# Kernel optimization log

Measured on AMD Instinct MI355X. Metric: run time of the kernel, lower is better.

Reference implementation:

```python
import jax, jax.numpy as jnp
import numpy as np

# ---- static config (matches init_kwargs) ----
B, N_CAMS, C, H, W = 2, 6, 256, 32, 88
BEV_H = BEV_W = 100
NQ = BEV_H * BEV_W
D_PILLAR = 4
HEADS = 8
LEVELS = 3
HEAD_DIM = C // HEADS
PC_RANGE = (-51.2, -51.2, -5.0, 51.2, 51.2, 3.0)
OGFH, OGFW = 256, 704


def _make_lidar2img():
    """Plausible lidar->image projection matrices (K @ [R|t]) for 6 ring cameras."""
    mats = np.zeros((B, N_CAMS, 4, 4), np.float32)
    K = np.array([[557.0, 0.0, OGFW / 2.0], [0.0, 557.0, OGFH / 2.0], [0.0, 0.0, 1.0]], np.float64)
    for b in range(B):
        for n in range(N_CAMS):
            yaw = 2.0 * np.pi * n / N_CAMS + 0.05 * b
            fwd = np.array([np.cos(yaw), np.sin(yaw), 0.0])
            right = np.array([np.sin(yaw), -np.cos(yaw), 0.0])
            down = np.array([0.0, 0.0, -1.0])
            R = np.stack([right, down, fwd])  # lidar -> camera axes
            cam_center = np.array([1.5 * np.cos(yaw), 1.5 * np.sin(yaw), 1.8])
            t = -R @ cam_center
            P = K @ np.concatenate([R, t[:, None]], axis=1)
            mats[b, n, :3, :] = P.astype(np.float32)
            mats[b, n, 3, 3] = 1.0
    return jnp.asarray(mats)


def setup_inputs() -> dict:
    key = jax.random.key(0)
    ks = jax.random.split(key, 16)
    s = 0.02
    return {
        'imgs': jax.random.normal(ks[0], (B, N_CAMS, C, H, W), jnp.float32),
        'lidar2img': _make_lidar2img(),
        'bev_query': jax.random.normal(ks[1], (NQ, 1, C), jnp.float32) * s,
        'bev_pos': jax.random.normal(ks[2], (1, NQ, C), jnp.float32) * s,
        'cams_embeds': jax.random.normal(ks[3], (N_CAMS, C), jnp.float32) * s,
        'level_embeds': jax.random.normal(ks[4], (LEVELS, C), jnp.float32) * s,
        'w_fpn': jax.random.normal(ks[5], (LEVELS, C, C), jnp.float32) * s,
        'b_fpn': jnp.zeros((LEVELS, C), jnp.float32),
        'w_value': jax.random.normal(ks[6], (C, C), jnp.float32) * s,
        'b_value': jnp.zeros((C,), jnp.float32),
        'w_off': jax.random.normal(ks[7], (C, HEADS * LEVELS * D_PILLAR * 2), jnp.float32) * s,
        'b_off': jax.random.normal(ks[8], (HEADS * LEVELS * D_PILLAR * 2,), jnp.float32) * 0.5,
        'w_attn': jax.random.normal(ks[9], (C, HEADS * LEVELS * D_PILLAR), jnp.float32) * s,
        'b_attn': jnp.zeros((HEADS * LEVELS * D_PILLAR,), jnp.float32),
        'w_out': jax.random.normal(ks[10], (C, C), jnp.float32) * s,
        'b_out': jnp.zeros((C,), jnp.float32),
        'w_ts1': jax.random.normal(ks[11], (C, C), jnp.float32) * s,
        'b_ts1': jnp.zeros((C,), jnp.float32),
        'w_ts2': jax.random.normal(ks[12], (C, C), jnp.float32) * s,
        'b_ts2': jnp.zeros((C,), jnp.float32),
    }


def _deform_sample(v, loc, h, w):
    """Bilinear sample (grid_sample, zero padding, align_corners=False).
    v: [N, heads, h*w, dh]; loc: [N, heads, Q, 2] normalized to [0,1]. -> [N, heads, Q, dh]"""
    x = loc[..., 0] * w - 0.5
    y = loc[..., 1] * h - 0.5
    x0 = jnp.floor(x)
    y0 = jnp.floor(y)
    out = jnp.zeros(v.shape[:2] + (loc.shape[2], v.shape[-1]), v.dtype)
    for dx in (0, 1):
        for dy in (0, 1):
            xi = x0 + dx
            yi = y0 + dy
            wgt = (1.0 - jnp.abs(x - xi)) * (1.0 - jnp.abs(y - yi))
            valid = (xi >= 0) & (xi < w) & (yi >= 0) & (yi < h)
            idx = (jnp.clip(yi, 0, h - 1) * w + jnp.clip(xi, 0, w - 1)).astype(jnp.int32)
            g = jnp.take_along_axis(v, idx[..., None], axis=2)
            out = out + g * (wgt * valid)[..., None]
    return out


def _forward(imgs, lidar2img, bev_query, bev_pos, cams_embeds, level_embeds,
             w_fpn, b_fpn, w_value, b_value, w_off, b_off, w_attn, b_attn,
             w_out, b_out, w_ts1, b_ts1, w_ts2, b_ts2):
    # ---- FPN: 3 levels at strides 1/2/4 with per-level 1x1 projection ----
    x = imgs.reshape(B * N_CAMS, C, H, W)
    feats, shapes = [], []
    cur = x
    for l in range(LEVELS):
        if l > 0:
            bn, c, h, w = cur.shape
            cur = cur.reshape(bn, c, h // 2, 2, w // 2, 2).mean(axis=(3, 5))
        f = jnp.einsum('bchw,cd->bdhw', cur, w_fpn[l]) + b_fpn[l][None, :, None, None]
        feats.append(f)
        shapes.append((f.shape[2], f.shape[3]))
    # ---- flatten levels + cam/level embeds: [N, sum_hw, B, C] ----
    flat = []
    for l, f in enumerate(feats):
        h, w = shapes[l]
        fl = jnp.transpose(f.reshape(B, N_CAMS, C, h * w), (1, 0, 3, 2))  # [N,B,hw,C]
        fl = fl + cams_embeds[:, None, None, :] + level_embeds[l][None, None, None, :]
        flat.append(fl)
    feat_flatten = jnp.transpose(jnp.concatenate(flat, axis=2), (0, 2, 1, 3))  # [N,sum_hw,B,C]

    # ---- 3D pillar reference points, normalized [0,1] ----
    zrange = PC_RANGE[5] - PC_RANGE[2]
    zs = jnp.linspace(0.5, zrange - 0.5, D_PILLAR) / zrange
    xs = (jnp.arange(BEV_W, dtype=jnp.float32) + 0.5) / BEV_W
    ys = (jnp.arange(BEV_H, dtype=jnp.float32) + 0.5) / BEV_H
    gy, gx = jnp.meshgrid(ys, xs, indexing='ij')
    ref2d = jnp.stack([gx.ravel(), gy.ravel()], axis=-1)  # [NQ,2]
    ref3d = jnp.concatenate([
        jnp.broadcast_to(ref2d[None], (D_PILLAR, NQ, 2)),
        jnp.broadcast_to(zs[:, None, None].astype(jnp.float32), (D_PILLAR, NQ, 1)),
    ], axis=-1)
    scale = jnp.array([PC_RANGE[3] - PC_RANGE[0], PC_RANGE[4] - PC_RANGE[1], zrange], jnp.float32)
    shift = jnp.array(PC_RANGE[:3], jnp.float32)
    xyz = ref3d * scale + shift
    homog = jnp.concatenate([xyz, jnp.ones((D_PILLAR, NQ, 1), jnp.float32)], axis=-1)

    # ---- point sampling: project to each camera, mask invalid pixels ----
    pts = jnp.einsum('bnij,dqj->nbqdi', lidar2img, homog)  # [N,B,NQ,D,4]
    eps = 1e-5
    depth = pts[..., 2]
    xy = pts[..., :2] / jnp.maximum(depth[..., None], eps)
    ref_cam = xy / jnp.array([OGFW, OGFH], jnp.float32)  # [N,B,NQ,D,2]
    bev_mask = ((depth > eps) & (ref_cam[..., 0] > 0) & (ref_cam[..., 0] < 1)
                & (ref_cam[..., 1] > 0) & (ref_cam[..., 1] < 1))  # [N,B,NQ,D]

    pos = bev_pos[0]  # [NQ,C]

    def sca(query, value, ref_b, mask_b):
        # query [NQ,C]; value [N,sum_hw,C]; ref_b [N,NQ,D,2]; mask_b [N,NQ,D]
        residual = query
        q = query + pos
        v = value @ w_value + b_value
        off = (q @ w_off + b_off).reshape(NQ, HEADS, LEVELS, D_PILLAR, 2)
        attn = jax.nn.softmax((q @ w_attn + b_attn).reshape(NQ, HEADS, LEVELS * D_PILLAR), axis=-1)
        attn = attn.reshape(NQ, HEADS, LEVELS, D_PILLAR)
        out = jnp.zeros((N_CAMS, NQ, HEADS, HEAD_DIM), q.dtype)
        start = 0
        for l, (h, w) in enumerate(shapes):
            hw = h * w
            v_l = jnp.transpose(v[:, start:start + hw].reshape(N_CAMS, hw, HEADS, HEAD_DIM), (0, 2, 1, 3))
            start += hw
            norm = jnp.array([w, h], q.dtype)
            loc = ref_b[:, :, None, :, :] + off[None, :, :, l] / norm  # [N,NQ,heads,D,2]
            loc = jnp.transpose(loc, (0, 2, 1, 3, 4)).reshape(N_CAMS, HEADS, NQ * D_PILLAR, 2)
            s = _deform_sample(v_l, loc, h, w).reshape(N_CAMS, HEADS, NQ, D_PILLAR, HEAD_DIM)
            out = out + jnp.einsum('nhqpd,qhp->nqhd', s, attn[:, :, l])
        out = out.reshape(N_CAMS, NQ, C)
        valid = mask_b.any(axis=-1)  # [N,NQ]
        slots = (out * valid[..., None].astype(out.dtype)).sum(axis=0)
        count = jnp.maximum(valid.sum(axis=0), 1).astype(out.dtype)[:, None]
        slots = slots / count
        return slots @ w_out + b_out + residual

    def tsblock(t):
        return jax.nn.relu(t @ w_ts1 + b_ts1) @ w_ts2 + b_ts2

    bq = jnp.transpose(bev_query, (1, 0, 2))[0]  # [NQ,C]
    groups = []
    ego = bq
    for b in range(B):
        val = feat_flatten[:, :, b, :]
        r = ref_cam[:, b]
        m = bev_mask[:, b]
        if b == 0:
            for _ in range(2):
                bq = tsblock(sca(bq, val, r, m))
            ego = bq
            groups.append(ego.reshape(C, BEV_W, BEV_H))
        else:
            nb = tsblock(sca(ego, val, r, m))
            groups.append(nb.reshape(C, BEV_W, BEV_H))
    bev_groups = jnp.stack(groups, axis=0)  # [B,C,BEV_W,BEV_H]
    return bq[None], bev_groups


def reference(imgs, lidar2img, bev_query, bev_pos, cams_embeds, level_embeds,
              w_fpn, b_fpn, w_value, b_value, w_off, b_off, w_attn, b_attn,
              w_out, b_out, w_ts1, b_ts1, w_ts2, b_ts2):
    return _forward(imgs, lidar2img, bev_query, bev_pos, cams_embeds, level_embeds,
                    w_fpn, b_fpn, w_value, b_value, w_off, b_off, w_attn, b_attn,
                    w_out, b_out, w_ts1, b_ts1, w_ts2, b_ts2)
```

## Files before the change

### kernel.cpp

```cpp
#include <hip/hip_runtime.h>
#include <math.h>

typedef __attribute__((ext_vector_type(8))) short bf16x8;
typedef __attribute__((ext_vector_type(4))) float f32x4;

__device__ __forceinline__ unsigned short f2bf(float x) {
  union { float f; unsigned int u; } v; v.f = x;
  unsigned int r = v.u + 0x7fffu + ((v.u >> 16) & 1u);
  return (unsigned short)(r >> 16);
}
__device__ __forceinline__ float bf2f(unsigned short b) {
  union { unsigned int u; float f; } v; v.u = ((unsigned int)b) << 16; return v.f;
}
__device__ __forceinline__ void split2(float x, unsigned short& h, unsigned short& l) {
  h = f2bf(x);
  l = f2bf(x - bf2f(h));
}
__device__ __forceinline__ int fsi(int q, int c) { return q * 256 + (c ^ ((q & 7) << 2)); }

__device__ __forceinline__ void ld16(const unsigned short* b, bf16x8* f) {
  const unsigned short* b1 = b + 2048;
  const unsigned short* b2 = b + 4096;
  const unsigned short* b3 = b + 6144;
  asm volatile(
    "global_load_dwordx4 %0, %16, off\n\t"
    "global_load_dwordx4 %1, %16, off offset:1024\n\t"
    "global_load_dwordx4 %2, %16, off offset:2048\n\t"
    "global_load_dwordx4 %3, %16, off offset:3072\n\t"
    "global_load_dwordx4 %4, %17, off\n\t"
    "global_load_dwordx4 %5, %17, off offset:1024\n\t"
    "global_load_dwordx4 %6, %17, off offset:2048\n\t"
    "global_load_dwordx4 %7, %17, off offset:3072\n\t"
    "global_load_dwordx4 %8, %18, off\n\t"
    "global_load_dwordx4 %9, %18, off offset:1024\n\t"
    "global_load_dwordx4 %10, %18, off offset:2048\n\t"
    "global_load_dwordx4 %11, %18, off offset:3072\n\t"
    "global_load_dwordx4 %12, %19, off\n\t"
    "global_load_dwordx4 %13, %19, off offset:1024\n\t"
    "global_load_dwordx4 %14, %19, off offset:2048\n\t"
    "global_load_dwordx4 %15, %19, off offset:3072\n\t"
    "s_waitcnt vmcnt(0)"
    : "=&v"(f[0]), "=&v"(f[1]), "=&v"(f[2]), "=&v"(f[3]),
      "=&v"(f[4]), "=&v"(f[5]), "=&v"(f[6]), "=&v"(f[7]),
      "=&v"(f[8]), "=&v"(f[9]), "=&v"(f[10]), "=&v"(f[11]),
      "=&v"(f[12]), "=&v"(f[13]), "=&v"(f[14]), "=&v"(f[15])
    : "v"(b), "v"(b1), "v"(b2), "v"(b3));
}

#define MFMA(a, b, c) __builtin_amdgcn_mfma_f32_16x16x32_bf16(a, b, c, 0, 0, 0)

__device__ __forceinline__ void gemm2tiles(
    const unsigned short* __restrict__ Wp, int tile0,
    int lane, int lk, int l15,
    const unsigned short (&AS)[2][32][32][8], f32x4 (&acc)[2][2])
{
  const unsigned short* base = Wp + ((size_t)(tile0 >> 1) * 16384) + (size_t)lane * 8;
  bf16x8 f[32];
  ld16(base, f);
  ld16(base + 8192, f + 16);
#pragma unroll
  for (int ks = 0; ks < 8; ++ks) {
    bf16x8 bqh0 = *(const bf16x8*)&AS[0][ks * 4 + lk][l15][0];
    bf16x8 bqh1 = *(const bf16x8*)&AS[0][ks * 4 + lk][16 + l15][0];
    bf16x8 bql0 = *(const bf16x8*)&AS[1][ks * 4 + lk][l15][0];
    bf16x8 bql1 = *(const bf16x8*)&AS[1][ks * 4 + lk][16 + l15][0];
    bf16x8 h0 = f[2 * ks], l0 = f[2 * ks + 1];
    bf16x8 h1 = f[16 + 2 * ks], l1 = f[17 + 2 * ks];
    acc[0][0] = MFMA(h0, bqh0, acc[0][0]);
    acc[0][0] = MFMA(h0, bql0, acc[0][0]);
    acc[0][0] = MFMA(l0, bqh0, acc[0][0]);
    acc[0][1] = MFMA(h0, bqh1, acc[0][1]);
    acc[0][1] = MFMA(h0, bql1, acc[0][1]);
    acc[0][1] = MFMA(l0, bqh1, acc[0][1]);
    acc[1][0] = MFMA(h1, bqh0, acc[1][0]);
    acc[1][0] = MFMA(h1, bql0, acc[1][0]);
    acc[1][0] = MFMA(l1, bqh0, acc[1][0]);
    acc[1][1] = MFMA(h1, bqh1, acc[1][1]);
    acc[1][1] = MFMA(h1, bql1, acc[1][1]);
    acc[1][1] = MFMA(l1, bqh1, acc[1][1]);
  }
}

__device__ __forceinline__ void gemm1tile(
    const unsigned short* __restrict__ Wp, int tile,
    int lane, int lk, int l15,
    const unsigned short (&AS)[2][32][32][8], f32x4 (&acc)[2])
{
  const unsigned short* base = Wp + ((size_t)(tile >> 1) * 16384) + (size_t)(tile & 1) * 8192 + (size_t)lane * 8;
  bf16x8 f[16];
  ld16(base, f);
#pragma unroll
  for (int ks = 0; ks < 8; ++ks) {
    bf16x8 bqh0 = *(const bf16x8*)&AS[0][ks * 4 + lk][l15][0];
    bf16x8 bqh1 = *(const bf16x8*)&AS[0][ks * 4 + lk][16 + l15][0];
    bf16x8 bql0 = *(const bf16x8*)&AS[1][ks * 4 + lk][l15][0];
    bf16x8 bql1 = *(const bf16x8*)&AS[1][ks * 4 + lk][16 + l15][0];
    bf16x8 eh = f[2 * ks], el = f[2 * ks + 1];
    acc[0] = MFMA(eh, bqh0, acc[0]);
    acc[0] = MFMA(eh, bql0, acc[0]);
    acc[0] = MFMA(el, bqh0, acc[0]);
    acc[1] = MFMA(eh, bqh1, acc[1]);
    acc[1] = MFMA(eh, bql1, acc[1]);
    acc[1] = MFMA(el, bqh1, acc[1]);
  }
}

__global__ __launch_bounds__(256) void pool2x2(const float* __restrict__ in, float* __restrict__ out,
                                               int h, int w, int total)
{
  int i = blockIdx.x * 256 + threadIdx.x;
  if (i >= total) return;
  int x = i % w; int r = i / w; int y = r % h; int ci = r / h;
  const float* p = in + (size_t)ci * (4 * h * w) + (size_t)(2 * y) * (2 * w) + 2 * x;
  out[i] = (p[0] + p[1] + p[2 * w] + p[2 * w + 1]) * 0.25f;
}

__global__ __launch_bounds__(256) void prep(
    const float* __restrict__ wo, const float* __restrict__ bo,
    const float* __restrict__ wa, const float* __restrict__ ba,
    const float* __restrict__ wout, const float* __restrict__ wts1, const float* __restrict__ wts2,
    const float* __restrict__ wfpn, const float* __restrict__ wval,
    const float* __restrict__ cams, const float* __restrict__ lev,
    const float* __restrict__ bfpn, const float* __restrict__ bval,
    unsigned short* __restrict__ wcatH, unsigned short* __restrict__ wcatL, float* __restrict__ bcat,
    unsigned short* __restrict__ woutH, unsigned short* __restrict__ woutL,
    unsigned short* __restrict__ wts1H, unsigned short* __restrict__ wts1L,
    unsigned short* __restrict__ w45H, unsigned short* __restrict__ w45L,
    unsigned short* __restrict__ wcombH, unsigned short* __restrict__ wcombL,
    float* __restrict__ e2)
{
  int bb = blockIdx.x, t = threadIdx.x;
  if (bb < 768) {
    int l = bb >> 8, i = bb & 255, j = t;
    const float* a = wfpn + ((size_t)l * 256 + i) * 256;
    float acc = 0.f;
    for (int k = 0; k < 256; ++k) acc = fmaf(a[k], wval[(size_t)k * 256 + j], acc);
    unsigned short h, lo; split2(acc, h, lo);
    size_t o = ((size_t)l * 256 + j) * 256 + i;
    wcombH[o] = h; wcombL[o] = lo;
  } else if (bb < 1056) {
    int i = (bb - 768) * 256 + t;
    int c = i >> 8, k = i & 255;
    float v = (c < 192) ? wo[k * 192 + c] : wa[k * 96 + (c - 192)];
    unsigned short h, l; split2(v, h, l);
    wcatH[i] = h; wcatL[i] = l;
    if (i < 288) bcat[i] = (i < 192) ? bo[i] : ba[i - 192];
  } else if (bb < 1312) {
    int i = (bb - 1056) * 256 + t;
    int nn = i >> 8, k = i & 255;
    float v = wout[(size_t)k * 256 + nn];
    unsigned short h, l; split2(v, h, l);
    woutH[i] = h; woutL[i] = l;
  } else if (bb < 1568) {
    int i = (bb - 1312) * 256 + t;
    int nn = i >> 8, k = i & 255;
    float v = wts1[(size_t)k * 256 + nn];
    unsigned short h, l; split2(v, h, l);
    wts1H[i] = h; wts1L[i] = l;
  } else if (bb < 1824) {
    int i = (bb - 1568) * 256 + t;
    int nn = i >> 8, k = i & 255;
    float v = wts2[(size_t)k * 256 + nn];
    unsigned short h, l; split2(v, h, l);
    w45H[i] = h; w45L[i] = l;
  } else if (bb < 2112) {
    int mp = bb - 1824;
    int k = t;
    float acc = 0.f;
    for (int j = 0; j < 256; ++j) {
      float wc = (mp < 192) ? wo[j * 192 + mp] : wa[j * 96 + (mp - 192)];
      acc = fmaf(wts2[(size_t)k * 256 + j], wc, acc);
    }
    unsigned short h, l; split2(acc, h, l);
    size_t o = (size_t)(256 + mp) * 256 + k;
    w45H[o] = h; w45L[o] = l;
  } else {
    int e = bb - 2112;
    int n = e / 3, l = e % 3, j = t;
    float acc = bval[j];
    for (int k = 0; k < 256; ++k) {
      float s = cams[n * 256 + k] + lev[l * 256 + k] + bfpn[l * 256 + k];
      acc = fmaf(s, wval[(size_t)k * 256 + j], acc);
    }
    e2[(size_t)e * 256 + j] = acc;
  }
}

__global__ __launch_bounds__(256) void relayout(
    const unsigned short* __restrict__ wcombH, const unsigned short* __restrict__ wcombL,
    const unsigned short* __restrict__ wcatH, const unsigned short* __restrict__ wcatL,
    const unsigned short* __restrict__ woutH, const unsigned short* __restrict__ woutL,
    const unsigned short* __restrict__ wts1H, const unsigned short* __restrict__ wts1L,
    const unsigned short* __restrict__ w45H, const unsigned short* __restrict__ w45L,
    unsigned short* __restrict__ wcombP, unsigned short* __restrict__ wcatP,
    unsigned short* __restrict__ woutP, unsigned short* __restrict__ wts1P,
    unsigned short* __restrict__ w45P)
{
  int bb = blockIdx.x, t = threadIdx.x;
  const unsigned short *H, *L; unsigned short* P; int tile;
  if (bb < 48)      { H = wcombH; L = wcombL; P = wcombP; tile = bb; }
  else if (bb < 66) { H = wcatH;  L = wcatL;  P = wcatP;  tile = bb - 48; }
  else if (bb < 82) { H = woutH;  L = woutL;  P = woutP;  tile = bb - 66; }
  else if (bb < 98) { H = wts1H;  L = wts1L;  P = wts1P;  tile = bb - 82; }
  else              { H = w45H;   L = w45L;   P = w45P;   tile = bb - 98; }
#pragma unroll
  for (int e = 0; e < 32; ++e) {
    int idx = t * 32 + e;
    int slot = idx >> 9;
    int lane = (idx >> 3) & 63;
    int j8 = idx & 7;
    int ks = slot >> 1, hl = slot & 1;
    int col = tile * 16 + (lane & 15);
    int k = ks * 32 + (lane >> 4) * 8 + j8;
    size_t dst = ((size_t)(tile >> 1) * 16384) + (size_t)(((tile & 1) << 4) + slot) * 512 + (size_t)lane * 8 + j8;
    P[dst] = (hl ? L : H)[(size_t)col * 256 + k];
  }
}

__global__ __launch_bounds__(512) void value_fused(
    const float* __restrict__ img0, const float* __restrict__ cur1, const float* __restrict__ cur2,
    const unsigned short* __restrict__ wcombP,
    const float* __restrict__ e2, float* __restrict__ V)
{
  __shared__ __align__(16) unsigned short AS[2][32][32][8];
  int t = threadIdx.x, wid = t >> 6, lane = t & 63, l15 = lane & 15, lk = lane >> 4;
  int bx = blockIdx.x, cam = blockIdx.y;
  int level, tb, hw; const float* src;
  if (bx < 88)       { level = 0; tb = bx;       hw = 2816; src = img0; }
  else if (bx < 110) { level = 1; tb = bx - 88;  hw = 704;  src = cur1; }
  else               { level = 2; tb = bx - 110; hw = 176;  src = cur2; }
  int p0 = tb * 32;
  const int LST[3] = {0, 2816, 3520};
  src += (size_t)cam * 256 * hw;

  {
    int f4g = t & 7, kb = t >> 3;
    bool full = (p0 + 32 <= hw);
#pragma unroll
    for (int j = 0; j < 4; ++j) {
      int k = kb + j * 64;
      const float* row = src + (size_t)k * hw;
      int p = p0 + 4 * f4g;
      float4 v;
      if (full) v = *(const float4*)(row + p);
      else {
        v.x = (p < hw) ? row[p] : 0.f;     v.y = (p + 1 < hw) ? row[p + 1] : 0.f;
        v.z = (p + 2 < hw) ? row[p + 2] : 0.f; v.w = (p + 3 < hw) ? row[p + 3] : 0.f;
      }
      int ch = k >> 3, ko = k & 7;
      unsigned short h, l;
      split2(v.x, h, l); AS[0][ch][4 * f4g + 0][ko] = h; AS[1][ch][4 * f4g + 0][ko] = l;
      split2(v.y, h, l); AS[0][ch][4 * f4g + 1][ko] = h; AS[1][ch][4 * f4g + 1][ko] = l;
      split2(v.z, h, l); AS[0][ch][4 * f4g + 2][ko] = h; AS[1][ch][4 * f4g + 2][ko] = l;
      split2(v.w, h, l); AS[0][ch][4 * f4g + 3][ko] = h; AS[1][ch][4 * f4g + 3][ko] = l;
    }
  }
  __syncthreads();

  f32x4 zed = {0.f, 0.f, 0.f, 0.f};
  f32x4 acc[2][2] = {{zed, zed}, {zed, zed}};
  gemm2tiles(wcombP, level * 16 + wid * 2, lane, lk, l15, AS, acc);
  __syncthreads();

  float* ASf = (float*)(&AS[0][0][0][0]);
  const float* bias = e2 + (size_t)(cam * 3 + level) * 256;
#pragma unroll
  for (int mf = 0; mf < 2; ++mf) {
    int chb = (wid * 2 + mf) * 16 + lk * 4;
    float4 b4 = *(const float4*)(bias + chb);
#pragma unroll
    for (int nf = 0; nf < 2; ++nf) {
      int q = nf * 16 + l15;
      float4 o;
      o.x = acc[mf][nf][0] + b4.x; o.y = acc[mf][nf][1] + b4.y;
      o.z = acc[mf][nf][2] + b4.z; o.w = acc[mf][nf][3] + b4.w;
      *(float4*)&ASf[fsi(q, chb)] = o;
    }
  }
  __syncthreads();
  float* Vb = V + ((size_t)cam * 3696 + LST[level] + p0) * 256;
#pragma unroll
  for (int j = 0; j < 4; ++j) {
    int g = t + j * 512;
    int q = g >> 6, c = (g & 63) * 4;
    if (p0 + q < hw)
      *(float4*)(Vb + (size_t)q * 256 + c) = *(const float4*)&ASf[fsi(q, c)];
  }
}

__global__ __launch_bounds__(512) void fused_iter(
    const float* __restrict__ slots, const float* __restrict__ qin,
    const float* __restrict__ pos2, const float* __restrict__ rowbias,
    const unsigned short* __restrict__ woutP, const unsigned short* __restrict__ wts1P,
    const unsigned short* __restrict__ w45P, const unsigned short* __restrict__ wcatP,
    const float* __restrict__ bout, const float* __restrict__ bts1,
    const float* __restrict__ bts2, const float* __restrict__ bcat,
    float* __restrict__ qout, float* __restrict__ outA, float* __restrict__ outB,
    float* __restrict__ qtmpA, float* __restrict__ qtmpB, int init)
{
  __shared__ __align__(16) unsigned short AS[2][32][32][8];
  __shared__ __align__(16) float RS[8192];
  int t = threadIdx.x, wid = t >> 6, lane = t & 63, l15 = lane & 15, lk = lane >> 4;
  int r0 = blockIdx.x * 32;
  f32x4 zed = {0.f, 0.f, 0.f, 0.f};

  {
    const float* base = init ? qin : slots;
#pragma unroll
    for (int j = 0; j < 4; ++j) {
      int g = t + j * 512;
      int q = g >> 6, c = (g & 63) * 4;
      int rq = r0 + q; if (rq > 9999) rq = 9999;
      float4 a = *(const float4*)(base + (size_t)rq * 256 + c);
      if (init) {
        if (pos2) {
          float4 p = *(const float4*)(pos2 + (size_t)rq * 256 + c);
          a.x += p.x; a.y += p.y; a.z += p.z; a.w += p.w;
        }
        if (rowbias) {
          float4 rb = *(const float4*)(rowbias + c);
          a.x += rb.x; a.y += rb.y; a.z += rb.z; a.w += rb.w;
        }
      }
      ushort4 hh, ll;
      split2(a.x, hh.x, ll.x); split2(a.y, hh.y, ll.y);
      split2(a.z, hh.z, ll.z); split2(a.w, hh.w, ll.w);
      *(ushort4*)&AS[0][c >> 3][q][c & 7] = hh;
      *(ushort4*)&AS[1][c >> 3][q][c & 7] = ll;
    }
    if (!init) {
#pragma unroll
      for (int j = 0; j < 4; ++j) {
        int g = t + j * 512;
        int q = g >> 6, c = (g & 63) * 4;
        int rq = r0 + q; if (rq > 9999) rq = 9999;
        *(float4*)&RS[fsi(q, c)] = *(const float4*)(qin + (size_t)rq * 256 + c);
      }
    }
  }
  __syncthreads();

  if (init) {
    f32x4 acc[2][2] = {{zed, zed}, {zed, zed}};
    gemm2tiles(wcatP, wid * 2, lane, lk, l15, AS, acc);
    f32x4 acc3[2] = {zed, zed};
    if (wid < 2) gemm1tile(wcatP, 16 + wid, lane, lk, l15, AS, acc3);
    __syncthreads();
    float* ASf = (float*)(&AS[0][0][0][0]);
#pragma unroll
    for (int mf = 0; mf < 2; ++mf) {
      int chb = (wid * 2 + mf) * 16 + lk * 4;
      float4 b4 = *(const float4*)(bcat + chb);
#pragma unroll
      for (int nf = 0; nf < 2; ++nf) {
        int q = nf * 16 + l15;
        float4 o;
        o.x = acc[mf][nf][0] + b4.x; o.y = acc[mf][nf][1] + b4.y;
        o.z = acc[mf][nf][2] + b4.z; o.w = acc[mf][nf][3] + b4.w;
        *(float4*)&ASf[fsi(q, chb)] = o;
      }
    }
    if (wid < 2) {
      int ce = wid * 16 + lk * 4;
      float4 b4 = *(const float4*)(bcat + 256 + ce);
#pragma unroll
      for (int nf = 0; nf < 2; ++nf) {
        int qg = r0 + nf * 16 + l15;
        if (qg < 10000) {
          float4 o;
          o.x = acc3[nf][0] + b4.x; o.y = acc3[nf][1] + b4.y;
          o.z = acc3[nf][2] + b4.z; o.w = acc3[nf][3] + b4.w;
          *(float4*)(qtmpB + (size_t)qg * 32 + ce) = o;
        }
      }
    }
    __syncthreads();
#pragma unroll
    for (int j = 0; j < 4; ++j) {
      int g = t + j * 512;
      int q = g >> 6, c = (g & 63) * 4;
      int qg = r0 + q;
      if (qg < 10000)
        *(float4*)(qtmpA + (size_t)qg * 256 + c) = *(const float4*)&ASf[fsi(q, c)];
    }
    return;
  }

  {
    f32x4 acc[2][2] = {{zed, zed}, {zed, zed}};
    gemm2tiles(woutP, wid * 2, lane, lk, l15, AS, acc);
    __syncthreads();
#pragma unroll
    for (int mf = 0; mf < 2; ++mf) {
      int chb = (wid * 2 + mf) * 16 + lk * 4;
      float4 b4 = *(const float4*)(bout + chb);
#pragma unroll
      for (int nf = 0; nf < 2; ++nf) {
        int q = nf * 16 + l15;
        float4 rr = *(const float4*)&RS[fsi(q, chb)];
        float v0 = acc[mf][nf][0] + b4.x + rr.x;
        float v1 = acc[mf][nf][1] + b4.y + rr.y;
        float v2 = acc[mf][nf][2] + b4.z + rr.z;
        float v3 = acc[mf][nf][3] + b4.w + rr.w;
        ushort4 hh, ll;
        split2(v0, hh.x, ll.x); split2(v1, hh.y, ll.y);
        split2(v2, hh.z, ll.z); split2(v3, hh.w, ll.w);
        *(ushort4*)&AS[0][chb >> 3][q][chb & 7] = hh;
        *(ushort4*)&AS[1][chb >> 3][q][chb & 7] = ll;
      }
    }
    __syncthreads();
  }
  {
    f32x4 acc[2][2] = {{zed, zed}, {zed, zed}};
    gemm2tiles(wts1P, wid * 2, lane, lk, l15, AS, acc);
    __syncthreads();
#pragma unroll
    for (int mf = 0; mf < 2; ++mf) {
      int chb = (wid * 2 + mf) * 16 + lk * 4;
      float4 b4 = *(const float4*)(bts1 + chb);
#pragma unroll
      for (int nf = 0; nf < 2; ++nf) {
        int q = nf * 16 + l15;
        float v0 = fmaxf(acc[mf][nf][0] + b4.x, 0.f);
        float v1 = fmaxf(acc[mf][nf][1] + b4.y, 0.f);
        float v2 = fmaxf(acc[mf][nf][2] + b4.z, 0.f);
        float v3 = fmaxf(acc[mf][nf][3] + b4.w, 0.f);
        ushort4 hh, ll;
        split2(v0, hh.x, ll.x); split2(v1, hh.y, ll.y);
        split2(v2, hh.z, ll.z); split2(v3, hh.w, ll.w);
        *(ushort4*)&AS[0][chb >> 3][q][chb & 7] = hh;
        *(ushort4*)&AS[1][chb >> 3][q][chb & 7] = ll;
      }
    }
    __syncthreads();
  }
  {
    f32x4 accA[2][2] = {{zed, zed}, {zed, zed}};
    f32x4 accB[2][2] = {{zed, zed}, {zed, zed}};
    if (wid < 4 || qtmpA) {
      gemm2tiles(w45P, wid * 4,     lane, lk, l15, AS, accA);
      gemm2tiles(w45P, wid * 4 + 2, lane, lk, l15, AS, accB);
    }
    f32x4 acc3[2] = {zed, zed};
    if (qtmpA && wid < 2) gemm1tile(w45P, 32 + wid, lane, lk, l15, AS, acc3);
    __syncthreads();
    float* ASf = (float*)(&AS[0][0][0][0]);
    if (wid < 4) {
#pragma unroll
      for (int half = 0; half < 2; ++half) {
#pragma unroll
        for (int mf = 0; mf < 2; ++mf) {
          int chb = (wid * 4 + half * 2 + mf) * 16 + lk * 4;
          float4 b4 = *(const float4*)(bts2 + chb);
#pragma unroll
          for (int nf = 0; nf < 2; ++nf) {
            int q = nf * 16 + l15;
            f32x4 a = half ? accB[mf][nf] : accA[mf][nf];
            float4 o;
            o.x = a[0] + b4.x; o.y = a[1] + b4.y;
            o.z = a[2] + b4.z; o.w = a[3] + b4.w;
            *(float4*)&RS[fsi(q, chb)] = o;
          }
        }
      }
    } else if (qtmpA) {
#pragma unroll
      for (int half = 0; half < 2; ++half) {
#pragma unroll
        for (int mf = 0; mf < 2; ++mf) {
          int cc = ((wid - 4) * 4 + half * 2 + mf) * 16 + lk * 4;
#pragma unroll
          for (int nf = 0; nf < 2; ++nf) {
            int q = nf * 16 + l15;
            f32x4 a = half ? accB[mf][nf] : accA[mf][nf];
            float4 o;
            o.x = a[0]; o.y = a[1]; o.z = a[2]; o.w = a[3];
            *(float4*)&ASf[fsi(q, cc)] = o;
          }
        }
      }
    }
    if (qtmpA && wid < 2) {
      int ce = wid * 16 + lk * 4;
#pragma unroll
      for (int nf = 0; nf < 2; ++nf) {
        int qg = r0 + nf * 16 + l15;
        if (qg < 10000) {
          float4 o;
          o.x = acc3[nf][0]; o.y = acc3[nf][1]; o.z = acc3[nf][2]; o.w = acc3[nf][3];
          *(float4*)(qtmpB + (size_t)qg * 32 + ce) = o;
        }
      }
    }
    __syncthreads();
#pragma unroll
    for (int j = 0; j < 4; ++j) {
      int g = t + j * 512;
      int q = g >> 6, c = (g & 63) * 4;
      int qg = r0 + q;
      if (qg < 10000) {
        float4 vq = *(const float4*)&RS[fsi(q, c)];
        size_t go = (size_t)qg * 256 + c;
        *(float4*)(qout + go) = vq;
        if (outA) { *(float4*)(outA + go) = vq; *(float4*)(outB + go) = vq; }
        if (qtmpA) *(float4*)(qtmpA + go) = *(const float4*)&ASf[fsi(q, c)];
      }
    }
  }
}

__global__ __launch_bounds__(256) void sca_sample(const float* __restrict__ qtmpA, const float* __restrict__ qtmpB,
                                                  const float* __restrict__ posA, const float* __restrict__ posB,
                                                  const float* __restrict__ V,
                                                  const float* __restrict__ l2i, float* __restrict__ slots)
{
  int b = blockIdx.x;
  int q = (b & 7) * 1250 + (b >> 3);
  int t = threadIdx.x;
  int head = t >> 5;
  __shared__ float raw[288];
  __shared__ float attnS[96];
  __shared__ float refx[6][4], refy[6][4];
  __shared__ int mnd[24];
  __shared__ int validn[6];
  __shared__ __align__(16) float w4[576][4];
  __shared__ __align__(16) int o4[576][4];

  {
    float x = qtmpA[(size_t)q * 256 + t];
    if (posA) x += posA[(size_t)q * 256 + t];
    raw[t] = x;
    if (t < 32) {
      float y = qtmpB[(size_t)q * 32 + t];
      if (posB) y += posB[(size_t)q * 32 + t];
      raw[256 + t] = y;
    }
  }
  if (t >= 32 && t < 56) {
    int tt = t - 32;
    int n = tt >> 2, d = tt & 3;
    const float* Mrow = l2i + n * 16;
    int qx = q % 100, qy = q / 100;
    float X = ((qx + 0.5f) / 100.0f) * 102.4f + (-51.2f);
    float Y = ((qy + 0.5f) / 100.0f) * 102.4f + (-51.2f);
    float zi = (d == 3) ? 7.5f : (0.5f + (float)d * (7.0f / 3.0f));
    float Z = zi + (-5.0f);
    float px = Mrow[0] * X + Mrow[1] * Y + Mrow[2] * Z + Mrow[3];
    float py = Mrow[4] * X + Mrow[5] * Y + Mrow[6] * Z + Mrow[7];
    float pz = Mrow[8] * X + Mrow[9] * Y + Mrow[10] * Z + Mrow[11];
    float dz = fmaxf(pz, 1e-5f);
    float xc = (px / dz) / 704.0f;
    float yc = (py / dz) / 256.0f;
    refx[n][d] = xc; refy[n][d] = yc;
    mnd[n * 4 + d] = (pz > 1e-5f) && (xc > 0.f) && (xc < 1.f) && (yc > 0.f) && (yc < 1.f);
  }
  __syncthreads();
  if (t < 8) {
    float mx = raw[192 + t * 12];
    for (int p = 1; p < 12; ++p) mx = fmaxf(mx, raw[192 + t * 12 + p]);
    float s = 0.f;
    float e[12];
#pragma unroll
    for (int p = 0; p < 12; ++p) { e[p] = __expf(raw[192 + t * 12 + p] - mx); s += e[p]; }
    float inv = 1.f / s;
#pragma unroll
    for (int p = 0; p < 12; ++p) attnS[t * 12 + p] = e[p] * inv;
  } else if (t < 14) {
    int n = t - 8;
    validn[n] = mnd[n * 4] | mnd[n * 4 + 1] | mnd[n * 4 + 2] | mnd[n * 4 + 3];
  }
  __syncthreads();

  int nv = validn[0] + validn[1] + validn[2] + validn[3] + validn[4] + validn[5];
  float invc = 1.f / (float)(nv > 1 ? nv : 1);

  const float WWf[3] = {88.f, 44.f, 22.f}, HHf[3] = {32.f, 16.f, 8.f};
  const int WWi[3] = {88, 44, 22}, STi[3] = {0, 2816, 3520};
  for (int pt = t; pt < 576; pt += 256) {
    int hd = pt & 7;
    int g = pt >> 3;
    int j = g % 12, n = g / 12;
    int l = j >> 2, d = j & 3;
    float wwf = WWf[l], hhf = HHf[l];
    int wwi = WWi[l], st = STi[l];
    float a = attnS[hd * 12 + j] * invc;
    float ox = raw[hd * 24 + l * 8 + d * 2 + 0];
    float oy = raw[hd * 24 + l * 8 + d * 2 + 1];
    float x = refx[n][d] * wwf + ox - 0.5f;
    float y = refy[n][d] * hhf + oy - 0.5f;
    float x0 = floorf(x), y0 = floorf(y);
    float fx = x - x0, fy = y - y0;
    float wx0 = 1.f - fx, wy0 = 1.f - fy;
    float vx0 = (x0 >= 0.f && x0 < wwf) ? 1.f : 0.f;
    float vx1 = (x0 + 1.f >= 0.f && x0 + 1.f < wwf) ? 1.f : 0.f;
    float vy0 = (y0 >= 0.f && y0 < hhf) ? 1.f : 0.f;
    float vy1 = (y0 + 1.f >= 0.f && y0 + 1.f < hhf) ? 1.f : 0.f;
    w4[pt][0] = a * wx0 * wy0 * vx0 * vy0;
    w4[pt][1] = a * fx * wy0 * vx1 * vy0;
    w4[pt][2] = a * wx0 * fy * vx0 * vy1;
    w4[pt][3] = a * fx * fy * vx1 * vy1;
    int ix0 = (int)fminf(fmaxf(x0, 0.f), wwf - 1.f);
    int ix1 = (int)fminf(fmaxf(x0 + 1.f, 0.f), wwf - 1.f);
    int iy0 = (int)fminf(fmaxf(y0, 0.f), hhf - 1.f);
    int iy1 = (int)fminf(fmaxf(y0 + 1.f, 0.f), hhf - 1.f);
    int rA = (st + iy0 * wwi) * 256, rB = (st + iy1 * wwi) * 256;
    o4[pt][0] = rA + ix0 * 256;
    o4[pt][1] = rA + ix1 * 256;
    o4[pt][2] = rB + ix0 * 256;
    o4[pt][3] = rB + ix1 * 256;
  }
  __syncthreads();

  float acc0 = 0.f, acc1 = 0.f;
#pragma unroll
  for (int n = 0; n < 6; ++n) {
    if (!validn[n]) continue;
    const float* Vn = V + (size_t)n * 946176 + t;
    int pb = n * 96 + head;
    float va[48];
#pragma unroll
    for (int j = 0; j < 12; ++j) {
      int4 o = *reinterpret_cast<const int4*>(&o4[pb + j * 8][0]);
      va[4 * j + 0] = Vn[o.x];
      va[4 * j + 1] = Vn[o.y];
      va[4 * j + 2] = Vn[o.z];
      va[4 * j + 3] = Vn[o.w];
    }
#pragma unroll
    for (int j = 0; j < 12; ++j) {
      float4 w = *reinterpret_cast<const float4*>(&w4[pb + j * 8][0]);
      acc0 = fmaf(w.x, va[4 * j + 0], acc0);
      acc1 = fmaf(w.y, va[4 * j + 1], acc1);
      acc0 = fmaf(w.z, va[4 * j + 2], acc0);
      acc1 = fmaf(w.w, va[4 * j + 3], acc1);
    }
  }
  slots[(size_t)q * 256 + t] = acc0 + acc1;
}

extern "C" void kernel_launch(void* const* d_in, const int* in_sizes, int n_in,
                              void* d_out, int out_size, void* d_ws, size_t ws_size,
                              hipStream_t stream)
{
  const float* imgs = (const float*)d_in[0];
  const float* l2i = (const float*)d_in[1];
  const float* bev_query = (const float*)d_in[2];
  const float* bev_pos = (const float*)d_in[3];
  const float* cams = (const float*)d_in[4];
  const float* lev = (const float*)d_in[5];
  const float* wfpn = (const float*)d_in[6];
  const float* bfpn = (const float*)d_in[7];
  const float* wval = (const float*)d_in[8];
  const float* bval = (const float*)d_in[9];
  const float* woff = (const float*)d_in[10];
  const float* boff = (const float*)d_in[11];
  const float* wattn = (const float*)d_in[12];
  const float* battn = (const float*)d_in[13];
  const float* wout = (const float*)d_in[14];
  const float* bout = (const float*)d_in[15];
  const float* wts1 = (const float*)d_in[16];
  const float* bts1 = (const float*)d_in[17];
  const float* wts2 = (const float*)d_in[18];
  const float* bts2 = (const float*)d_in[19];

  float* W = (float*)d_ws;
  size_t off = 0;
  auto alloc = [&](size_t n) { float* p = W + off; off += n; return p; };
  float* v    = alloc((size_t)6 * 3696 * 256);
  float* cur1 = alloc((size_t)12 * 256 * 16 * 44);
  float* cur2 = alloc((size_t)12 * 256 * 8 * 22);
  float* bqA  = alloc(2560000);
  float* bqB  = alloc(2560000);
  float* qtmpA = alloc(2560000);
  float* qtmpB = alloc(320000);
  float* posA = alloc(2560000);
  float* posB = alloc(320000);
  float* slots = alloc(2560000);
  float* wcatR = alloc(73728);
  float* woutR = alloc(65536);
  float* wts1R = alloc(65536);
  float* w45R = alloc(139264);
  float* wcombR = alloc(196608);
  float* wcombPR = alloc(196608);
  float* wcatPR = alloc(73728);
  float* woutPR = alloc(65536);
  float* wts1PR = alloc(65536);
  float* w45PR = alloc(139264);
  float* bcat = alloc(512);
  float* e2 = alloc(4608);
  (void)ws_size; (void)in_sizes; (void)n_in; (void)out_size;

  unsigned short* wcat_h = (unsigned short*)wcatR;   unsigned short* wcat_l = wcat_h + 288 * 256;
  unsigned short* wout_h = (unsigned short*)woutR;   unsigned short* wout_l = wout_h + 65536;
  unsigned short* wts1_h = (unsigned short*)wts1R;   unsigned short* wts1_l = wts1_h + 65536;
  unsigned short* w45_h = (unsigned short*)w45R;     unsigned short* w45_l = w45_h + 544 * 256;
  unsigned short* wcomb_h = (unsigned short*)wcombR; unsigned short* wcomb_l = wcomb_h + 3 * 65536;
  unsigned short* wcombP = (unsigned short*)wcombPR;
  unsigned short* wcatP = (unsigned short*)wcatPR;
  unsigned short* woutP = (unsigned short*)woutPR;
  unsigned short* wts1P = (unsigned short*)wts1PR;
  unsigned short* w45P = (unsigned short*)w45PR;

  float* OUT = (float*)d_out;

  pool2x2<<<8448, 256, 0, stream>>>(imgs, cur1, 16, 44, 2162688);
  pool2x2<<<2112, 256, 0, stream>>>(cur1, cur2, 8, 22, 540672);
  prep<<<2130, 256, 0, stream>>>(woff, boff, wattn, battn, wout, wts1, wts2, wfpn, wval,
                                 cams, lev, bfpn, bval,
                                 wcat_h, wcat_l, bcat, wout_h, wout_l, wts1_h, wts1_l,
                                 w45_h, w45_l, wcomb_h, wcomb_l, e2);
  relayout<<<132, 256, 0, stream>>>(wcomb_h, wcomb_l, wcat_h, wcat_l, wout_h, wout_l,
                                    wts1_h, wts1_l, w45_h, w45_l,
                                    wcombP, wcatP, woutP, wts1P, w45P);

  fused_iter<<<313, 512, 0, stream>>>(nullptr, bev_pos, nullptr, bts2,
      woutP, wts1P, w45P, wcatP, bout, bts1, bts2, bcat,
      nullptr, nullptr, nullptr, posA, posB, 1);
  fused_iter<<<313, 512, 0, stream>>>(nullptr, bev_query, bev_pos, nullptr,
      woutP, wts1P, w45P, wcatP, bout, bts1, bts2, bcat,
      nullptr, nullptr, nullptr, qtmpA, qtmpB, 1);

  value_fused<<<dim3(116, 6), 512, 0, stream>>>(imgs, cur1, cur2, wcombP, e2, v);

  sca_sample<<<10000, 256, 0, stream>>>(qtmpA, qtmpB, nullptr, nullptr, v, l2i, slots);
  fused_iter<<<313, 512, 0, stream>>>(slots, bev_query, nullptr, nullptr,
      woutP, wts1P, w45P, wcatP, bout, bts1, bts2, bcat,
      bqA, nullptr, nullptr, qtmpA, qtmpB, 0);
  sca_sample<<<10000, 256, 0, stream>>>(qtmpA, qtmpB, posA, posB, v, l2i, slots);
  fused_iter<<<313, 512, 0, stream>>>(slots, bqA, nullptr, nullptr,
      woutP, wts1P, w45P, wcatP, bout, bts1, bts2, bcat,
      bqB, OUT, OUT + 2560000, qtmpA, qtmpB, 0);

  value_fused<<<dim3(116, 6), 512, 0, stream>>>(imgs + (size_t)4325376, cur1 + (size_t)1081344,
                                                cur2 + (size_t)270336, wcombP, e2, v);
  sca_sample<<<10000, 256, 0, stream>>>(qtmpA, qtmpB, posA, posB, v, l2i + 96, slots);
  fused_iter<<<313, 512, 0, stream>>>(slots, bqB, nullptr, nullptr,
      woutP, wts1P, w45P, wcatP, bout, bts1, bts2, bcat,
      OUT + 5120000, nullptr, nullptr, nullptr, nullptr, 0);
}
```

Baseline: 334.9 us.

## Double fused_iter row tile to 64 queries and drop separate residual LDS buffer

fused_iter now processes 64 BEV queries per block instead of 32, so each weight fragment loaded from global memory is reused across four query sub-tiles, roughly halving weight traffic per query. To fit the larger activation tile in shared memory, the separate RS residual buffer is removed. The residual rows are loaded into registers after the first GEMM and staged through the shared activation buffer, and the output and qtmp writes are reordered around extra barriers. The grid drops from 313 to 157 blocks, which leaves fewer blocks than the GPU's compute units and adds accumulator register pressure.

```diff
diff --git a/kernel.cpp b/kernel.cpp
--- a/kernel.cpp
+++ b/kernel.cpp
@@ -49,7 +49,7 @@
 
 #define MFMA(a, b, c) __builtin_amdgcn_mfma_f32_16x16x32_bf16(a, b, c, 0, 0, 0)
 
-__device__ __forceinline__ void gemm2tiles(
+__device__ __forceinline__ void gemm2t32(
     const unsigned short* __restrict__ Wp, int tile0,
     int lane, int lk, int l15,
     const unsigned short (&AS)[2][32][32][8], f32x4 (&acc)[2][2])
@@ -60,48 +60,68 @@
   ld16(base + 8192, f + 16);
 #pragma unroll
   for (int ks = 0; ks < 8; ++ks) {
-    bf16x8 bqh0 = *(const bf16x8*)&AS[0][ks * 4 + lk][l15][0];
-    bf16x8 bqh1 = *(const bf16x8*)&AS[0][ks * 4 + lk][16 + l15][0];
-    bf16x8 bql0 = *(const bf16x8*)&AS[1][ks * 4 + lk][l15][0];
-    bf16x8 bql1 = *(const bf16x8*)&AS[1][ks * 4 + lk][16 + l15][0];
     bf16x8 h0 = f[2 * ks], l0 = f[2 * ks + 1];
     bf16x8 h1 = f[16 + 2 * ks], l1 = f[17 + 2 * ks];
-    acc[0][0] = MFMA(h0, bqh0, acc[0][0]);
-    acc[0][0] = MFMA(h0, bql0, acc[0][0]);
-    acc[0][0] = MFMA(l0, bqh0, acc[0][0]);
-    acc[0][1] = MFMA(h0, bqh1, acc[0][1]);
-    acc[0][1] = MFMA(h0, bql1, acc[0][1]);
-    acc[0][1] = MFMA(l0, bqh1, acc[0][1]);
-    acc[1][0] = MFMA(h1, bqh0, acc[1][0]);
-    acc[1][0] = MFMA(h1, bql0, acc[1][0]);
-    acc[1][0] = MFMA(l1, bqh0, acc[1][0]);
-    acc[1][1] = MFMA(h1, bqh1, acc[1][1]);
-    acc[1][1] = MFMA(h1, bql1, acc[1][1]);
-    acc[1][1] = MFMA(l1, bqh1, acc[1][1]);
-  }
-}
-
-__device__ __forceinline__ void gemm1tile(
+#pragma unroll
+    for (int nf = 0; nf < 2; ++nf) {
+      bf16x8 bqh = *(const bf16x8*)&AS[0][ks * 4 + lk][nf * 16 + l15][0];
+      bf16x8 bql = *(const bf16x8*)&AS[1][ks * 4 + lk][nf * 16 + l15][0];
+      acc[0][nf] = MFMA(h0, bqh, acc[0][nf]);
+      acc[0][nf] = MFMA(h0, bql, acc[0][nf]);
+      acc[0][nf] = MFMA(l0, bqh, acc[0][nf]);
+      acc[1][nf] = MFMA(h1, bqh, acc[1][nf]);
+      acc[1][nf] = MFMA(h1, bql, acc[1][nf]);
+      acc[1][nf] = MFMA(l1, bqh, acc[1][nf]);
+    }
+  }
+}
+
+__device__ __forceinline__ void gemm2t64(
+    const unsigned short* __restrict__ Wp, int tile0,
+    int lane, int lk, int l15,
+    const unsigned short (&AS)[2][32][64][8], f32x4 (&acc)[2][4])
+{
+  const unsigned short* base = Wp + ((size_t)(tile0 >> 1) * 16384) + (size_t)lane * 8;
+  bf16x8 f[32];
+  ld16(base, f);
+  ld16(base + 8192, f + 16);
+#pragma unroll
+  for (int ks = 0; ks < 8; ++ks) {
+    bf16x8 h0 = f[2 * ks], l0 = f[2 * ks + 1];
+    bf16x8 h1 = f[16 + 2 * ks], l1 = f[17 + 2 * ks];
+#pragma unroll
+    for (int nf = 0; nf < 4; ++nf) {
+      bf16x8 bqh = *(const bf16x8*)&AS[0][ks * 4 + lk][nf * 16 + l15][0];
+      bf16x8 bql = *(const bf16x8*)&AS[1][ks * 4 + lk][nf * 16 + l15][0];
+      acc[0][nf] = MFMA(h0, bqh, acc[0][nf]);
+      acc[0][nf] = MFMA(h0, bql, acc[0][nf]);
+      acc[0][nf] = MFMA(l0, bqh, acc[0][nf]);
+      acc[1][nf] = MFMA(h1, bqh, acc[1][nf]);
+      acc[1][nf] = MFMA(h1, bql, acc[1][nf]);
+      acc[1][nf] = MFMA(l1, bqh, acc[1][nf]);
+    }
+  }
+}
+
+__device__ __forceinline__ void gemm1t64(
     const unsigned short* __restrict__ Wp, int tile,
     int lane, int lk, int l15,
-    const unsigned short (&AS)[2][32][32][8], f32x4 (&acc)[2])
+    const unsigned short (&AS)[2][32][64][8], f32x4 (&acc)[4])
 {
   const unsigned short* base = Wp + ((size_t)(tile >> 1) * 16384) + (size_t)(tile & 1) * 8192 + (size_t)lane * 8;
   bf16x8 f[16];
   ld16(base, f);
 #pragma unroll
   for (int ks = 0; ks < 8; ++ks) {
-    bf16x8 bqh0 = *(const bf16x8*)&AS[0][ks * 4 + lk][l15][0];
-    bf16x8 bqh1 = *(const bf16x8*)&AS[0][ks * 4 + lk][16 + l15][0];
-    bf16x8 bql0 = *(const bf16x8*)&AS[1][ks * 4 + lk][l15][0];
-    bf16x8 bql1 = *(const bf16x8*)&AS[1][ks * 4 + lk][16 + l15][0];
     bf16x8 eh = f[2 * ks], el = f[2 * ks + 1];
-    acc[0] = MFMA(eh, bqh0, acc[0]);
-    acc[0] = MFMA(eh, bql0, acc[0]);
-    acc[0] = MFMA(el, bqh0, acc[0]);
-    acc[1] = MFMA(eh, bqh1, acc[1]);
-    acc[1] = MFMA(eh, bql1, acc[1]);
-    acc[1] = MFMA(el, bqh1, acc[1]);
+#pragma unroll
+    for (int nf = 0; nf < 4; ++nf) {
+      bf16x8 bqh = *(const bf16x8*)&AS[0][ks * 4 + lk][nf * 16 + l15][0];
+      bf16x8 bql = *(const bf16x8*)&AS[1][ks * 4 + lk][nf * 16 + l15][0];
+      acc[nf] = MFMA(eh, bqh, acc[nf]);
+      acc[nf] = MFMA(eh, bql, acc[nf]);
+      acc[nf] = MFMA(el, bqh, acc[nf]);
+    }
   }
 }
 
@@ -259,7 +279,7 @@
 
   f32x4 zed = {0.f, 0.f, 0.f, 0.f};
   f32x4 acc[2][2] = {{zed, zed}, {zed, zed}};
-  gemm2tiles(wcombP, level * 16 + wid * 2, lane, lk, l15, AS, acc);
+  gemm2t32(wcombP, level * 16 + wid * 2, lane, lk, l15, AS, acc);
   __syncthreads();
 
   float* ASf = (float*)(&AS[0][0][0][0]);
@@ -298,16 +318,16 @@
     float* __restrict__ qout, float* __restrict__ outA, float* __restrict__ outB,
     float* __restrict__ qtmpA, float* __restrict__ qtmpB, int init)
 {
-  __shared__ __align__(16) unsigned short AS[2][32][32][8];
-  __shared__ __align__(16) float RS[8192];
+  __shared__ __align__(16) unsigned short AS[2][32][64][8];
+  float* ASf = (float*)(&AS[0][0][0][0]);
   int t = threadIdx.x, wid = t >> 6, lane = t & 63, l15 = lane & 15, lk = lane >> 4;
-  int r0 = blockIdx.x * 32;
+  int r0 = blockIdx.x * 64;
   f32x4 zed = {0.f, 0.f, 0.f, 0.f};
 
   {
     const float* base = init ? qin : slots;
 #pragma unroll
-    for (int j = 0; j < 4; ++j) {
+    for (int j = 0; j < 8; ++j) {
       int g = t + j * 512;
       int q = g >> 6, c = (g & 63) * 4;
       int rq = r0 + q; if (rq > 9999) rq = 9999;
@@ -328,31 +348,21 @@
       *(ushort4*)&AS[0][c >> 3][q][c & 7] = hh;
       *(ushort4*)&AS[1][c >> 3][q][c & 7] = ll;
     }
-    if (!init) {
-#pragma unroll
-      for (int j = 0; j < 4; ++j) {
-        int g = t + j * 512;
-        int q = g >> 6, c = (g & 63) * 4;
-        int rq = r0 + q; if (rq > 9999) rq = 9999;
-        *(float4*)&RS[fsi(q, c)] = *(const float4*)(qin + (size_t)rq * 256 + c);
-      }
-    }
   }
   __syncthreads();
 
   if (init) {
-    f32x4 acc[2][2] = {{zed, zed}, {zed, zed}};
-    gemm2tiles(wcatP, wid * 2, lane, lk, l15, AS, acc);
-    f32x4 acc3[2] = {zed, zed};
-    if (wid < 2) gemm1tile(wcatP, 16 + wid, lane, lk, l15, AS, acc3);
-    __syncthreads();
-    float* ASf = (float*)(&AS[0][0][0][0]);
+    f32x4 acc[2][4] = {{zed, zed, zed, zed}, {zed, zed, zed, zed}};
+    gemm2t64(wcatP, wid * 2, lane, lk, l15, AS, acc);
+    f32x4 acc3[4] = {zed, zed, zed, zed};
+    if (wid < 2) gemm1t64(wcatP, 16 + wid, lane, lk, l15, AS, acc3);
+    __syncthreads();
 #pragma unroll
     for (int mf = 0; mf < 2; ++mf) {
       int chb = (wid * 2 + mf) * 16 + lk * 4;
       float4 b4 = *(const float4*)(bcat + chb);
 #pragma unroll
-      for (int nf = 0; nf < 2; ++nf) {
+      for (int nf = 0; nf < 4; ++nf) {
         int q = nf * 16 + l15;
         float4 o;
         o.x = acc[mf][nf][0] + b4.x; o.y = acc[mf][nf][1] + b4.y;
@@ -364,7 +374,7 @@
       int ce = wid * 16 + lk * 4;
       float4 b4 = *(const float4*)(bcat + 256 + ce);
 #pragma unroll
-      for (int nf = 0; nf < 2; ++nf) {
+      for (int nf = 0; nf < 4; ++nf) {
         int qg = r0 + nf * 16 + l15;
         if (qg < 10000) {
           float4 o;
@@ -376,7 +386,7 @@
     }
     __syncthreads();
 #pragma unroll
-    for (int j = 0; j < 4; ++j) {
+    for (int j = 0; j < 8; ++j) {
       int g = t + j * 512;
       int q = g >> 6, c = (g & 63) * 4;
       int qg = r0 + q;
@@ -387,21 +397,44 @@
   }
 
   {
-    f32x4 acc[2][2] = {{zed, zed}, {zed, zed}};
-    gemm2tiles(woutP, wid * 2, lane, lk, l15, AS, acc);
+    f32x4 acc[2][4] = {{zed, zed, zed, zed}, {zed, zed, zed, zed}};
+    gemm2t64(woutP, wid * 2, lane, lk, l15, AS, acc);
+    __syncthreads();
+    float4 qreg[8];
+#pragma unroll
+    for (int j = 0; j < 8; ++j) {
+      int g = t + j * 512;
+      int q = g >> 6, c = (g & 63) * 4;
+      int rq = r0 + q; if (rq > 9999) rq = 9999;
+      qreg[j] = *(const float4*)(qin + (size_t)rq * 256 + c);
+    }
+#pragma unroll
+    for (int j = 0; j < 8; ++j) {
+      int g = t + j * 512;
+      int q = g >> 6, c = (g & 63) * 4;
+      *(float4*)&ASf[fsi(q, c)] = qreg[j];
+    }
+    __syncthreads();
+    float4 rr[2][4];
+#pragma unroll
+    for (int mf = 0; mf < 2; ++mf) {
+      int chb = (wid * 2 + mf) * 16 + lk * 4;
+#pragma unroll
+      for (int nf = 0; nf < 4; ++nf)
+        rr[mf][nf] = *(const float4*)&ASf[fsi(nf * 16 + l15, chb)];
+    }
     __syncthreads();
 #pragma unroll
     for (int mf = 0; mf < 2; ++mf) {
       int chb = (wid * 2 + mf) * 16 + lk * 4;
       float4 b4 = *(const float4*)(bout + chb);
 #pragma unroll
-      for (int nf = 0; nf < 2; ++nf) {
+      for (int nf = 0; nf < 4; ++nf) {
         int q = nf * 16 + l15;
-        float4 rr = *(const float4*)&RS[fsi(q, chb)];
-        float v0 = acc[mf][nf][0] + b4.x + rr.x;
-        float v1 = acc[mf][nf][1] + b4.y + rr.y;
-        float v2 = acc[mf][nf][2] + b4.z + rr.z;
-        float v3 = acc[mf][nf][3] + b4.w + rr.w;
+        float v0 = acc[mf][nf][0] + b4.x + rr[mf][nf].x;
+        float v1 = acc[mf][nf][1] + b4.y + rr[mf][nf].y;
+        float v2 = acc[mf][nf][2] + b4.z + rr[mf][nf].z;
+        float v3 = acc[mf][nf][3] + b4.w + rr[mf][nf].w;
         ushort4 hh, ll;
         split2(v0, hh.x, ll.x); split2(v1, hh.y, ll.y);
         split2(v2, hh.z, ll.z); split2(v3, hh.w, ll.w);
@@ -412,15 +445,15 @@
     __syncthreads();
   }
   {
-    f32x4 acc[2][2] = {{zed, zed}, {zed, zed}};
-    gemm2tiles(wts1P, wid * 2, lane, lk, l15, AS, acc);
+    f32x4 acc[2][4] = {{zed, zed, zed, zed}, {zed, zed, zed, zed}};
+    gemm2t64(wts1P, wid * 2, lane, lk, l15, AS, acc);
     __syncthreads();
 #pragma unroll
     for (int mf = 0; mf < 2; ++mf) {
       int chb = (wid * 2 + mf) * 16 + lk * 4;
       float4 b4 = *(const float4*)(bts1 + chb);
 #pragma unroll
-      for (int nf = 0; nf < 2; ++nf) {
+      for (int nf = 0; nf < 4; ++nf) {
         int q = nf * 16 + l15;
         float v0 = fmaxf(acc[mf][nf][0] + b4.x, 0.f);
         float v1 = fmaxf(acc[mf][nf][1] + b4.y, 0.f);
@@ -436,16 +469,15 @@
     __syncthreads();
   }
   {
-    f32x4 accA[2][2] = {{zed, zed}, {zed, zed}};
-    f32x4 accB[2][2] = {{zed, zed}, {zed, zed}};
+    f32x4 accA[2][4] = {{zed, zed, zed, zed}, {zed, zed, zed, zed}};
+    f32x4 accB[2][4] = {{zed, zed, zed, zed}, {zed, zed, zed, zed}};
     if (wid < 4 || qtmpA) {
-      gemm2tiles(w45P, wid * 4,     lane, lk, l15, AS, accA);
-      gemm2tiles(w45P, wid * 4 + 2, lane, lk, l15, AS, accB);
-    }
-    f32x4 acc3[2] = {zed, zed};
-    if (qtmpA && wid < 2) gemm1tile(w45P, 32 + wid, lane, lk, l15, AS, acc3);
-    __syncthreads();
-    float* ASf = (float*)(&AS[0][0][0][0]);
+      gemm2t64(w45P, wid * 4,     lane, lk, l15, AS, accA);
+      gemm2t64(w45P, wid * 4 + 2, lane, lk, l15, AS, accB);
+    }
+    f32x4 acc3[4] = {zed, zed, zed, zed};
+    if (qtmpA && wid < 2) gemm1t64(w45P, 32 + wid, lane, lk, l15, AS, acc3);
+    __syncthreads();
     if (wid < 4) {
 #pragma unroll
       for (int half = 0; half < 2; ++half) {
@@ -454,24 +486,52 @@
           int chb = (wid * 4 + half * 2 + mf) * 16 + lk * 4;
           float4 b4 = *(const float4*)(bts2 + chb);
 #pragma unroll
-          for (int nf = 0; nf < 2; ++nf) {
+          for (int nf = 0; nf < 4; ++nf) {
             int q = nf * 16 + l15;
             f32x4 a = half ? accB[mf][nf] : accA[mf][nf];
             float4 o;
             o.x = a[0] + b4.x; o.y = a[1] + b4.y;
             o.z = a[2] + b4.z; o.w = a[3] + b4.w;
-            *(float4*)&RS[fsi(q, chb)] = o;
+            *(float4*)&ASf[fsi(q, chb)] = o;
           }
         }
       }
-    } else if (qtmpA) {
+    }
+    if (qtmpA && wid < 2) {
+      int ce = wid * 16 + lk * 4;
+#pragma unroll
+      for (int nf = 0; nf < 4; ++nf) {
+        int qg = r0 + nf * 16 + l15;
+        if (qg < 10000) {
+          float4 o;
+          o.x = acc3[nf][0]; o.y = acc3[nf][1]; o.z = acc3[nf][2]; o.w = acc3[nf][3];
+          *(float4*)(qtmpB + (size_t)qg * 32 + ce) = o;
+        }
+      }
+    }
+    __syncthreads();
+#pragma unroll
+    for (int j = 0; j < 8; ++j) {
+      int g = t + j * 512;
+      int q = g >> 6, c = (g & 63) * 4;
+      int qg = r0 + q;
+      if (qg < 10000) {
+        float4 vq = *(const float4*)&ASf[fsi(q, c)];
+        size_t go = (size_t)qg * 256 + c;
+        *(float4*)(qout + go) = vq;
+        if (outA) { *(float4*)(outA + go) = vq; *(float4*)(outB + go) = vq; }
+      }
+    }
+    if (!qtmpA) return;
+    __syncthreads();
+    if (wid >= 4) {
 #pragma unroll
       for (int half = 0; half < 2; ++half) {
 #pragma unroll
         for (int mf = 0; mf < 2; ++mf) {
           int cc = ((wid - 4) * 4 + half * 2 + mf) * 16 + lk * 4;
 #pragma unroll
-          for (int nf = 0; nf < 2; ++nf) {
+          for (int nf = 0; nf < 4; ++nf) {
             int q = nf * 16 + l15;
             f32x4 a = half ? accB[mf][nf] : accA[mf][nf];
             float4 o;
@@ -481,31 +541,14 @@
         }
       }
     }
-    if (qtmpA && wid < 2) {
-      int ce = wid * 16 + lk * 4;
-#pragma unroll
-      for (int nf = 0; nf < 2; ++nf) {
-        int qg = r0 + nf * 16 + l15;
-        if (qg < 10000) {
-          float4 o;
-          o.x = acc3[nf][0]; o.y = acc3[nf][1]; o.z = acc3[nf][2]; o.w = acc3[nf][3];
-          *(float4*)(qtmpB + (size_t)qg * 32 + ce) = o;
-        }
-      }
-    }
-    __syncthreads();
-#pragma unroll
-    for (int j = 0; j < 4; ++j) {
+    __syncthreads();
+#pragma unroll
+    for (int j = 0; j < 8; ++j) {
       int g = t + j * 512;
       int q = g >> 6, c = (g & 63) * 4;
       int qg = r0 + q;
-      if (qg < 10000) {
-        float4 vq = *(const float4*)&RS[fsi(q, c)];
-        size_t go = (size_t)qg * 256 + c;
-        *(float4*)(qout + go) = vq;
-        if (outA) { *(float4*)(outA + go) = vq; *(float4*)(outB + go) = vq; }
-        if (qtmpA) *(float4*)(qtmpA + go) = *(const float4*)&ASf[fsi(q, c)];
-      }
+      if (qg < 10000)
+        *(float4*)(qtmpA + (size_t)qg * 256 + c) = *(const float4*)&ASf[fsi(q, c)];
     }
   }
 }
@@ -714,28 +757,28 @@
                                     wts1_h, wts1_l, w45_h, w45_l,
                                     wcombP, wcatP, woutP, wts1P, w45P);
 
-  fused_iter<<<313, 512, 0, stream>>>(nullptr, bev_pos, nullptr, bts2,
+  fused_iter<<<157, 512, 0, stream>>>(nullptr, bev_pos, nullptr, bts2,
       woutP, wts1P, w45P, wcatP, bout, bts1, bts2, bcat,
       nullptr, nullptr, nullptr, posA, posB, 1);
-  fused_iter<<<313, 512, 0, stream>>>(nullptr, bev_query, bev_pos, nullptr,
+  fused_iter<<<157, 512, 0, stream>>>(nullptr, bev_query, bev_pos, nullptr,
       woutP, wts1P, w45P, wcatP, bout, bts1, bts2, bcat,
       nullptr, nullptr, nullptr, qtmpA, qtmpB, 1);
 
   value_fused<<<dim3(116, 6), 512, 0, stream>>>(imgs, cur1, cur2, wcombP, e2, v);
 
   sca_sample<<<10000, 256, 0, stream>>>(qtmpA, qtmpB, nullptr, nullptr, v, l2i, slots);
-  fused_iter<<<313, 512, 0, stream>>>(slots, bev_query, nullptr, nullptr,
+  fused_iter<<<157, 512, 0, stream>>>(slots, bev_query, nullptr, nullptr,
       woutP, wts1P, w45P, wcatP, bout, bts1, bts2, bcat,
       bqA, nullptr, nullptr, qtmpA, qtmpB, 0);
   sca_sample<<<10000, 256, 0, stream>>>(qtmpA, qtmpB, posA, posB, v, l2i, slots);
-  fused_iter<<<313, 512, 0, stream>>>(slots, bqA, nullptr, nullptr,
+  fused_iter<<<157, 512, 0, stream>>>(slots, bqA, nullptr, nullptr,
       woutP, wts1P, w45P, wcatP, bout, bts1, bts2, bcat,
       bqB, OUT, OUT + 2560000, qtmpA, qtmpB, 0);
 
   value_fused<<<dim3(116, 6), 512, 0, stream>>>(imgs + (size_t)4325376, cur1 + (size_t)1081344,
                                                 cur2 + (size_t)270336, wcombP, e2, v);
   sca_sample<<<10000, 256, 0, stream>>>(qtmpA, qtmpB, posA, posB, v, l2i + 96, slots);
-  fused_iter<<<313, 512, 0, stream>>>(slots, bqB, nullptr, nullptr,
+  fused_iter<<<157, 512, 0, stream>>>(slots, bqB, nullptr, nullptr,
       woutP, wts1P, w45P, wcatP, bout, bts1, bts2, bcat,
       OUT + 5120000, nullptr, nullptr, nullptr, nullptr, 0);
 }
```

New measurement: 320.7 us. -4.3%, faster.
